# Performance work log

Measured on AMD Instinct MI355X. Metric: run time of the kernel, lower is better.

Reference implementation:

```python
import jax, jax.numpy as jnp
import numpy as np

B, S, H, E, V, OOV = 64, 400, 512, 256, 50000, 100

def setup_inputs() -> dict:
    key = jax.random.key(0)
    ks = jax.random.split(key, 32)
    p = lambda i, shape: jax.random.normal(ks[i], shape, jnp.float32) * 0.02
    emb = p(0, (V, E)).at[0].set(0.0)  # padding_idx=0
    return dict(
        summaries_in=jax.random.randint(ks[1], (B,), 1, V),
        h0=jax.random.normal(ks[2], (B, H), jnp.float32),
        c0=jax.random.normal(ks[3], (B, H), jnp.float32),
        encoder_out=jax.random.normal(ks[4], (B, S, 2 * H), jnp.float32),
        encoder_features=jax.random.normal(ks[5], (S * B, 2 * H), jnp.float32),
        encoder_mask=jnp.ones((S, B), jnp.float32),
        context=jax.random.normal(ks[6], (B, 2 * H), jnp.float32),
        coverage=jax.random.uniform(ks[7], (S, B), jnp.float32) * 0.01,
        texts_extended=jax.random.randint(ks[8], (S, B), 0, V + OOV),
        oov_size=OOV,
        emb=emb,
        W_feat=p(10, (2 * H, 2 * H)), b_feat=p(11, (2 * H,)),
        W_cov=p(12, (2 * H,)), b_cov=p(13, (2 * H,)),
        w_att=p(14, (2 * H,)), b_att=p(15, ()),
        W_ih=p(16, (4 * H, E)), W_hh=p(17, (4 * H, H)),
        b_ih=p(18, (4 * H,)), b_hh=p(19, (4 * H,)),
        W_ctx=p(20, (E, 2 * H + E)), b_ctx=p(21, (E,)),
        W_pg=p(22, (4 * H + E,)), b_pg=p(23, ()),
        W_o1=p(24, (H, 3 * H)), b_o1=p(25, (H,)),
        W_o2=p(26, (V, H)), b_o2=p(27, (V,)),
    )


def reference(summaries_in, h0, c0, encoder_out, encoder_features, encoder_mask,
              context, coverage, texts_extended, oov_size, emb,
              W_feat, b_feat, W_cov, b_cov, w_att, b_att,
              W_ih, W_hh, b_ih, b_hh, W_ctx, b_ctx, W_pg, b_pg,
              W_o1, b_o1, W_o2, b_o2):
    # embedding + context projection: [B, 2H+E] -> [B, E]
    x = emb[summaries_in]
    ctx_out = jnp.concatenate([context, x], axis=1) @ W_ctx.T + b_ctx
    # single LSTM step (torch gate order i, f, g, o)
    gates = ctx_out @ W_ih.T + b_ih + h0 @ W_hh.T + b_hh
    i, f, g, o = jnp.split(gates, 4, axis=1)
    c = jax.nn.sigmoid(f) * c0 + jax.nn.sigmoid(i) * jnp.tanh(g)
    h = jax.nn.sigmoid(o) * jnp.tanh(c)
    hidden_out = jnp.concatenate([h, c], axis=1)  # [B, 2H]
    # Bahdanau attention with coverage
    dec_feat = hidden_out @ W_feat.T + b_feat                 # [B, 2H]
    ef = encoder_features.reshape(S, B, 2 * H)                # [S, B, 2H]
    cov_feat = coverage[..., None] * W_cov + b_cov            # Linear(1, 2H)
    e = jnp.tanh(ef + dec_feat[None] + cov_feat) @ w_att + b_att  # [S, B]
    a = jax.nn.softmax(e, axis=0) * encoder_mask
    a = a / jnp.sum(a, axis=0, keepdims=True)                 # renormalize (Normalize(0))
    ctx_new = jnp.einsum('sb,bsd->bd', a, encoder_out)        # [B, 2H]
    coverage_next = coverage + a
    # pointer-generator mix
    gen_in = jnp.concatenate([ctx_new, hidden_out, ctx_out], axis=1)  # [B, 4H+E]
    p_gen = jax.nn.sigmoid(gen_in @ W_pg + b_pg)[:, None]             # [B, 1]
    logits = (jnp.concatenate([h, ctx_new], axis=1) @ W_o1.T + b_o1) @ W_o2.T + b_o2
    vocab_dist = p_gen * jax.nn.softmax(logits, axis=1)       # [B, V]
    attn_w = (1.0 - p_gen) * a.T                              # [B, S]
    vd = jnp.concatenate([vocab_dist, jnp.zeros((B, oov_size), vocab_dist.dtype)], axis=1)
    vd = vd.at[jnp.arange(B)[:, None], texts_extended.T].add(attn_w)  # scatter_add copy dist
    return vd, hidden_out, ctx_new, a, coverage_next
```

## Files before the change

kernel.cpp:

```cpp
#include <hip/hip_runtime.h>
#include <cmath>

#define B 64
#define S 400
#define H 512
#define E 256
#define V 50000
#define OOV 100
#define H2 1024
#define VDN (V + OOV)
#define NBLK_V 782
#define SC 40

typedef __attribute__((ext_vector_type(8))) short short8;
typedef __attribute__((ext_vector_type(4))) float f32x4;

__device__ __forceinline__ float wred_sum(float v) {
#pragma unroll
  for (int o = 32; o > 0; o >>= 1) v += __shfl_down(v, o, 64);
  return v;
}
__device__ __forceinline__ float wred_max(float v) {
#pragma unroll
  for (int o = 32; o > 0; o >>= 1) v = fmaxf(v, __shfl_down(v, o, 64));
  return v;
}
__device__ __forceinline__ short f2bf(float f) {
  return __builtin_bit_cast(short, (__bf16)f);
}

__global__ __launch_bounds__(256) void k_pre(
    const float* __restrict__ b_ctx, const float* __restrict__ b_ih,
    const float* __restrict__ b_hh, const float* __restrict__ b_feat,
    const float* __restrict__ b_o1, const float* __restrict__ context,
    const float* __restrict__ emb, const int* __restrict__ sumin,
    const float* __restrict__ h0, float* __restrict__ ctxoutT4,
    float* __restrict__ gates, float* __restrict__ dfeat,
    float* __restrict__ innerT4, float* __restrict__ catT4,
    float* __restrict__ h0T4) {
  int idx = blockIdx.x * 256 + threadIdx.x;
  if (idx < 16384) {
    int j = ((idx >> 8) << 2) + (idx & 3);
    ctxoutT4[idx] = b_ctx[j];
  } else if (idx < 16384 + 131072) {
    int i = idx - 16384;
    int j = i & 2047;
    gates[i] = b_ih[j] + b_hh[j];
  } else if (idx < 16384 + 131072 + 65536) {
    int i = idx - 16384 - 131072;
    dfeat[i] = b_feat[i & 1023];
  } else if (idx < 245760) {
    int i = idx - 16384 - 131072 - 65536;
    int j = ((i >> 8) << 2) + (i & 3);
    innerT4[i] = b_o1[j];
  } else if (idx < 245760 + 81920) {
    int i = idx - 245760;
    int e = i & 3, b = (i >> 2) & 63, q = i >> 8;
    int k = q * 4 + e;
    catT4[i] = (k < 1024) ? context[b * 1024 + k]
                          : emb[(size_t)sumin[b] * 256 + (k - 1024)];
  } else {
    int i = idx - 245760 - 81920;
    int e = i & 3, b = (i >> 2) & 63, q = i >> 8;
    h0T4[i] = h0[b * 512 + q * 4 + e];
  }
}

template <int R, int KC, int OUTMODE>
__global__ __launch_bounds__(256) void k_gemmsk(
    const float* __restrict__ A1, const float* __restrict__ W1, int ldw1, int s1,
    const float* __restrict__ A2, const float* __restrict__ W2, int ldw2,
    float* __restrict__ out, int ldout) {
  const int lane = threadIdx.x;
  const int w = threadIdx.y;
  const int j0 = blockIdx.x * (4 * R) + w * R;
  const float* A;
  const float* W;
  int ldw, kc0;
  if ((int)blockIdx.y < s1) {
    A = A1; W = W1; ldw = ldw1; kc0 = blockIdx.y * KC;
  } else {
    A = A2; W = W2; ldw = ldw2; kc0 = (blockIdx.y - s1) * KC;
  }
  float acc[R];
#pragma unroll
  for (int r = 0; r < R; ++r) acc[r] = 0.f;
  const float* ap = A + (size_t)kc0 * 256 + lane * 4;
  const float* wr[R];
#pragma unroll
  for (int r = 0; r < R; ++r) wr[r] = W + (size_t)(j0 + r) * ldw + kc0 * 4;
#pragma unroll 8
  for (int k4 = 0; k4 < KC; ++k4) {
    float4 av = *(const float4*)(ap + (size_t)k4 * 256);
#pragma unroll
    for (int r = 0; r < R; ++r) {
      float4 wv = *(const float4*)(wr[r] + k4 * 4);
      acc[r] += av.x * wv.x + av.y * wv.y + av.z * wv.z + av.w * wv.w;
    }
  }
#pragma unroll
  for (int r = 0; r < R; ++r) {
    int j = j0 + r;
    if constexpr (OUTMODE == 0)
      atomicAdd(&out[((size_t)(j >> 2) * 64 + lane) * 4 + (j & 3)], acc[r]);
    else
      atomicAdd(&out[(size_t)lane * ldout + j], acc[r]);
  }
}

__global__ __launch_bounds__(256) void k_lstm(const float* __restrict__ gates,
                                              const float* __restrict__ c0,
                                              float* __restrict__ hidden,
                                              float* __restrict__ hcT4) {
  int idx = blockIdx.x * 256 + threadIdx.x;
  int b = idx >> 9, u = idx & 511;
  float gi = gates[(size_t)b * 2048 + u];
  float gf = gates[(size_t)b * 2048 + 512 + u];
  float gg = gates[(size_t)b * 2048 + 1024 + u];
  float go = gates[(size_t)b * 2048 + 1536 + u];
  float si = 1.f / (1.f + expf(-gi));
  float sf = 1.f / (1.f + expf(-gf));
  float so = 1.f / (1.f + expf(-go));
  float c = sf * c0[(size_t)b * 512 + u] + si * tanhf(gg);
  float h = so * tanhf(c);
  hidden[(size_t)b * H2 + u] = h;
  hidden[(size_t)b * H2 + 512 + u] = c;
  hcT4[((u >> 2) * 64 + b) * 4 + (u & 3)] = h;
  int k = 512 + u;
  hcT4[((k >> 2) * 64 + b) * 4 + (k & 3)] = c;
}

__global__ __launch_bounds__(256) void k_e(
    const float* __restrict__ ef, const float* __restrict__ dfeat,
    const float* __restrict__ cov, const float* __restrict__ Wcov,
    const float* __restrict__ bcov, const float* __restrict__ watt,
    const float* __restrict__ batt, float* __restrict__ e_out) {
  const int t = threadIdx.x;
  const int r = t >> 5;
  const int li = t & 31;
  const int sb = blockIdx.x * 8 + r;
  const int b = sb & 63;
  const float cval = cov[sb];
  const float4* efr = (const float4*)(ef + (size_t)sb * H2);
  const float4* dfr = (const float4*)(dfeat + (size_t)b * H2);
  const float4* wcr = (const float4*)Wcov;
  const float4* bcr = (const float4*)bcov;
  const float4* war = (const float4*)watt;
  float sum = 0.f;
#pragma unroll
  for (int i = 0; i < 8; ++i) {
    int d4 = li + i * 32;
    float4 ev = efr[d4], dv = dfr[d4], wc = wcr[d4], bc = bcr[d4], wa = war[d4];
    sum += tanhf(ev.x + dv.x + cval * wc.x + bc.x) * wa.x;
    sum += tanhf(ev.y + dv.y + cval * wc.y + bc.y) * wa.y;
    sum += tanhf(ev.z + dv.z + cval * wc.z + bc.z) * wa.z;
    sum += tanhf(ev.w + dv.w + cval * wc.w + bc.w) * wa.w;
  }
#pragma unroll
  for (int o = 16; o > 0; o >>= 1) sum += __shfl_down(sum, o, 32);
  if (li == 0) e_out[sb] = sum + batt[0];
}

__global__ __launch_bounds__(512) void k_soft(const float* __restrict__ e,
                                              const float* __restrict__ mask,
                                              const float* __restrict__ cov_in,
                                              float* __restrict__ a_out,
                                              float* __restrict__ cov_out) {
  const int b = blockIdx.x;
  const int s = threadIdx.x;
  __shared__ float red[8];
  float ev = (s < S) ? e[s * B + b] : -INFINITY;
  float m = wred_max(ev);
  if ((s & 63) == 0) red[s >> 6] = m;
  __syncthreads();
  if (s == 0) {
    float mm = red[0];
#pragma unroll
    for (int i = 1; i < 8; ++i) mm = fmaxf(mm, red[i]);
    red[0] = mm;
  }
  __syncthreads();
  m = red[0];
  float ex = (s < S) ? mask[s * B + b] * expf(ev - m) : 0.f;
  float ws = wred_sum(ex);
  __syncthreads();
  if ((s & 63) == 0) red[s >> 6] = ws;
  __syncthreads();
  if (s == 0) {
    float z = 0.f;
#pragma unroll
    for (int i = 0; i < 8; ++i) z += red[i];
    red[0] = z;
  }
  __syncthreads();
  float Z = red[0];
  if (s < S) {
    float av = ex / Z;
    a_out[s * B + b] = av;
    cov_out[s * B + b] = cov_in[s * B + b] + av;
  }
}

__global__ __launch_bounds__(256) void k_ctxp(const float* __restrict__ a,
                                              const float* __restrict__ enc,
                                              float* __restrict__ part) {
  const int b = blockIdx.x & 63;
  const int sc = blockIdx.x >> 6;
  const int d = threadIdx.x * 4;
  float4 acc = make_float4(0.f, 0.f, 0.f, 0.f);
#pragma unroll
  for (int i = 0; i < 10; ++i) {
    int s = sc * 10 + i;
    float av = a[s * B + b];
    float4 ev = *(const float4*)(enc + ((size_t)b * S + s) * H2 + d);
    acc.x += av * ev.x;
    acc.y += av * ev.y;
    acc.z += av * ev.z;
    acc.w += av * ev.w;
  }
  *(float4*)(part + (size_t)blockIdx.x * H2 + d) = acc;
}

__global__ __launch_bounds__(256) void k_ctxred(const float* __restrict__ part,
                                                float* __restrict__ ctx_new,
                                                float* __restrict__ ctxT4) {
  int idx = blockIdx.x * 256 + threadIdx.x;
  float s = 0.f;
#pragma unroll
  for (int sc = 0; sc < SC; ++sc) s += part[(size_t)sc * 65536 + idx];
  int b = idx >> 10, d = idx & 1023;
  ctx_new[idx] = s;
  ctxT4[((d >> 2) * 64 + b) * 4 + (d & 3)] = s;
}

__global__ __launch_bounds__(256) void k_pgen(
    const float* __restrict__ ctx_new, const float* __restrict__ hidden,
    const float* __restrict__ ctxoutT4, const float* __restrict__ Wpg,
    const float* __restrict__ bpg, float* __restrict__ pgen) {
  const int b = blockIdx.x;
  float p = 0.f;
  for (int k = threadIdx.x; k < 2304; k += 256) {
    float v;
    if (k < 1024) v = ctx_new[(size_t)b * H2 + k];
    else if (k < 2048) v = hidden[(size_t)b * H2 + k - 1024];
    else {
      int ko = k - 2048;
      v = ctxoutT4[((ko >> 2) * 64 + b) * 4 + (ko & 3)];
    }
    p += v * Wpg[k];
  }
  p = wred_sum(p);
  __shared__ float red[4];
  if ((threadIdx.x & 63) == 0) red[threadIdx.x >> 6] = p;
  __syncthreads();
  if (threadIdx.x == 0) {
    float d = red[0] + red[1] + red[2] + red[3] + bpg[0];
    pgen[b] = 1.f / (1.f + expf(-d));
  }
}

__global__ __launch_bounds__(256) void k_packinner(const float* __restrict__ innerT4,
                                                   short8* __restrict__ packB) {
  int f = blockIdx.x * 256 + threadIdx.x;
  int l = f & 63, bt = (f >> 6) & 3, ks = f >> 8;
  int b = bt * 16 + (l & 15);
  int kbase = ks * 32 + (l >> 4) * 8;
  float4 q0 = *(const float4*)&innerT4[(size_t)(kbase / 4) * 256 + b * 4];
  float4 q1 = *(const float4*)&innerT4[(size_t)(kbase / 4 + 1) * 256 + b * 4];
  short8 frag;
  frag[0] = f2bf(q0.x); frag[1] = f2bf(q0.y);
  frag[2] = f2bf(q0.z); frag[3] = f2bf(q0.w);
  frag[4] = f2bf(q1.x); frag[5] = f2bf(q1.y);
  frag[6] = f2bf(q1.z); frag[7] = f2bf(q1.w);
  packB[f] = frag;
}

__global__ __launch_bounds__(256) void k_mfma_logits(
    const float* __restrict__ W2, const short8* __restrict__ packB,
    const float* __restrict__ bias, float* __restrict__ logits,
    float* __restrict__ mp, float* __restrict__ zp) {
  const int l = threadIdx.x;
  const int w = threadIdx.y;
  const int jblk = blockIdx.x * 64;
  const int jw = jblk + w * 16;
  const int jv = min(jw + (l & 15), V - 1);
  const float4* wp4 = (const float4*)(W2 + (size_t)jv * 512 + (l >> 4) * 8);

  f32x4 acc0 = {0.f, 0.f, 0.f, 0.f}, acc1 = acc0, acc2 = acc0, acc3 = acc0;
  float4 cw0 = wp4[0], cw1 = wp4[1];
#pragma unroll
  for (int ks = 0; ks < 16; ++ks) {
    float4 nw0, nw1;
    if (ks < 15) { nw0 = wp4[(ks + 1) * 8]; nw1 = wp4[(ks + 1) * 8 + 1]; }
    short8 af;
    af[0] = f2bf(cw0.x); af[1] = f2bf(cw0.y); af[2] = f2bf(cw0.z); af[3] = f2bf(cw0.w);
    af[4] = f2bf(cw1.x); af[5] = f2bf(cw1.y); af[6] = f2bf(cw1.z); af[7] = f2bf(cw1.w);
    short8 b0 = packB[(ks * 4 + 0) * 64 + l];
    short8 b1 = packB[(ks * 4 + 1) * 64 + l];
    short8 b2 = packB[(ks * 4 + 2) * 64 + l];
    short8 b3 = packB[(ks * 4 + 3) * 64 + l];
    acc0 = __builtin_amdgcn_mfma_f32_16x16x32_bf16(af, b0, acc0, 0, 0, 0);
    acc1 = __builtin_amdgcn_mfma_f32_16x16x32_bf16(af, b1, acc1, 0, 0, 0);
    acc2 = __builtin_amdgcn_mfma_f32_16x16x32_bf16(af, b2, acc2, 0, 0, 0);
    acc3 = __builtin_amdgcn_mfma_f32_16x16x32_bf16(af, b3, acc3, 0, 0, 0);
    if (ks < 15) { cw0 = nw0; cw1 = nw1; }
  }

  __shared__ float tile[64][65];
  const int rbase = w * 16 + (l >> 4) * 4;
#pragma unroll
  for (int v = 0; v < 4; ++v) {
    int jl = rbase + v;
    int j = jblk + jl;
    float bv = bias[min(j, V - 1)];
    bool valid = (j < V);
    tile[jl][0 * 16 + (l & 15)] = valid ? acc0[v] + bv : -INFINITY;
    tile[jl][1 * 16 + (l & 15)] = valid ? acc1[v] + bv : -INFINITY;
    tile[jl][2 * 16 + (l & 15)] = valid ? acc2[v] + bv : -INFINITY;
    tile[jl][3 * 16 + (l & 15)] = valid ? acc3[v] + bv : -INFINITY;
  }
  __syncthreads();
  const int t = w * 64 + l;
#pragma unroll
  for (int i = 0; i < 16; ++i) {
    int idx = i * 256 + t;
    int jl = idx & 63;
    int b = idx >> 6;
    int j = jblk + jl;
    if (j < V) logits[(size_t)b * V + j] = tile[jl][b];
  }
  if (t < 64) {
    float m = -INFINITY;
#pragma unroll
    for (int jl = 0; jl < 64; ++jl) m = fmaxf(m, tile[jl][t]);
    float z = 0.f;
#pragma unroll
    for (int jl = 0; jl < 64; ++jl) z += expf(tile[jl][t] - m);
    mp[(size_t)blockIdx.x * 64 + t] = m;
    zp[(size_t)blockIdx.x * 64 + t] = z;
  }
}

__global__ __launch_bounds__(256) void k_vdm(const float* __restrict__ logits,
                                             const float* __restrict__ mp,
                                             const float* __restrict__ zp,
                                             const float* __restrict__ pgen,
                                             float* __restrict__ out) {
  const int b = blockIdx.x >> 3;
  const int c = blockIdx.x & 7;
  const int t = threadIdx.x;
  __shared__ float red[4];
  float m = -INFINITY;
  for (int i = t; i < NBLK_V; i += 256) m = fmaxf(m, mp[i * 64 + b]);
  m = wred_max(m);
  if ((t & 63) == 0) red[t >> 6] = m;
  __syncthreads();
  const float M = fmaxf(fmaxf(red[0], red[1]), fmaxf(red[2], red[3]));
  float z = 0.f;
  for (int i = t; i < NBLK_V; i += 256) z += zp[i * 64 + b] * expf(mp[i * 64 + b] - M);
  z = wred_sum(z);
  __syncthreads();
  if ((t & 63) == 0) red[t >> 6] = z;
  __syncthreads();
  const float Z = red[0] + red[1] + red[2] + red[3];
  const float scale = pgen[b] / Z;
  const int v0 = c * 6272;
  const int v1 = min(v0 + 6272, VDN);
  for (int v = v0 + t; v < v1; v += 256) {
    float val = (v < V) ? scale * expf(logits[(size_t)b * V + v] - M) : 0.f;
    out[(size_t)b * VDN + v] = val;
  }
}

__global__ __launch_bounds__(256) void k_scatter(const float* __restrict__ a,
                                                 const int* __restrict__ tex,
                                                 const float* __restrict__ pgen,
                                                 float* __restrict__ vd) {
  int g = blockIdx.x * 256 + threadIdx.x;
  if (g >= S * B) return;
  int b = g & 63;
  float w = (1.f - pgen[b]) * a[g];
  atomicAdd(&vd[(size_t)b * VDN + tex[g]], w);
}

extern "C" void kernel_launch(void* const* d_in, const int* in_sizes, int n_in,
                              void* d_out, int out_size, void* d_ws, size_t ws_size,
                              hipStream_t stream) {
  const int* sumin = (const int*)d_in[0];
  const float* h0 = (const float*)d_in[1];
  const float* c0 = (const float*)d_in[2];
  const float* enc_out = (const float*)d_in[3];
  const float* ef = (const float*)d_in[4];
  const float* mask = (const float*)d_in[5];
  const float* context = (const float*)d_in[6];
  const float* coverage = (const float*)d_in[7];
  const int* tex = (const int*)d_in[8];
  const float* emb = (const float*)d_in[10];
  const float* W_feat = (const float*)d_in[11];
  const float* b_feat = (const float*)d_in[12];
  const float* W_cov = (const float*)d_in[13];
  const float* b_cov = (const float*)d_in[14];
  const float* w_att = (const float*)d_in[15];
  const float* b_att = (const float*)d_in[16];
  const float* W_ih = (const float*)d_in[17];
  const float* W_hh = (const float*)d_in[18];
  const float* b_ih = (const float*)d_in[19];
  const float* b_hh = (const float*)d_in[20];
  const float* W_ctx = (const float*)d_in[21];
  const float* b_ctx = (const float*)d_in[22];
  const float* W_pg = (const float*)d_in[23];
  const float* b_pg = (const float*)d_in[24];
  const float* W_o1 = (const float*)d_in[25];
  const float* b_o1 = (const float*)d_in[26];
  const float* W_o2 = (const float*)d_in[27];
  const float* b_o2 = (const float*)d_in[28];

  float* out = (float*)d_out;
  float* vd = out;
  float* hidden = vd + (size_t)B * VDN;
  float* ctx_new = hidden + (size_t)B * H2;
  float* a_out = ctx_new + (size_t)B * H2;
  float* cov_out = a_out + (size_t)S * B;

  float* ws = (float*)d_ws;
  float* catT4 = ws;
  float* h0T4 = catT4 + 81920;
  float* ctxoutT4 = h0T4 + 32768;
  float* gates = ctxoutT4 + 16384;
  float* hidcatT4 = gates + 131072;
  float* dfeat = hidcatT4 + 65536;
  float* e_ws = dfeat + 65536;
  float* ctxnewT4 = e_ws + 25600;
  float* innerT4 = ctxnewT4 + 65536;
  float* pgen = innerT4 + 32768;
  float* mp = pgen + 64;
  float* zp = mp + 50048;
  float* packBf = zp + 50048;
  float* logits = packBf + 16384;
  float* part = logits;
  short8* packB = (short8*)packBf;

  dim3 gblk(64, 4);

  k_pre<<<1408, 256, 0, stream>>>(b_ctx, b_ih, b_hh, b_feat, b_o1, context, emb,
                                  sumin, h0, ctxoutT4, gates, dfeat, innerT4,
                                  catT4, h0T4);
  k_gemmsk<2, 64, 0><<<dim3(32, 5), gblk, 0, stream>>>(
      catT4, W_ctx, 1280, 5, nullptr, nullptr, 0, ctxoutT4, 0);
  k_gemmsk<2, 64, 1><<<dim3(256, 3), gblk, 0, stream>>>(
      ctxoutT4, W_ih, 256, 1, h0T4, W_hh, 512, gates, 2048);
  k_lstm<<<128, 256, 0, stream>>>(gates, c0, hidden, hidcatT4);
  k_gemmsk<2, 64, 1><<<dim3(128, 4), gblk, 0, stream>>>(
      hidcatT4, W_feat, 1024, 4, nullptr, nullptr, 0, dfeat, 1024);
  k_e<<<3200, 256, 0, stream>>>(ef, dfeat, coverage, W_cov, b_cov, w_att, b_att,
                                e_ws);
  k_soft<<<B, 512, 0, stream>>>(e_ws, mask, coverage, a_out, cov_out);
  k_ctxp<<<SC * B, 256, 0, stream>>>(a_out, enc_out, part);
  k_ctxred<<<256, 256, 0, stream>>>(part, ctx_new, ctxnewT4);
  k_pgen<<<B, 256, 0, stream>>>(ctx_new, hidden, ctxoutT4, W_pg, b_pg, pgen);
  k_gemmsk<2, 64, 0><<<dim3(64, 6), gblk, 0, stream>>>(
      hidcatT4, W_o1, 1536, 2, ctxnewT4, W_o1 + 512, 1536, innerT4, 0);
  k_packinner<<<16, 256, 0, stream>>>(innerT4, packB);
  k_mfma_logits<<<NBLK_V, gblk, 0, stream>>>(W_o2, packB, b_o2, logits, mp, zp);
  k_vdm<<<B * 8, 256, 0, stream>>>(logits, mp, zp, pgen, vd);
  k_scatter<<<100, 256, 0, stream>>>(a_out, tex, pgen, vd);
}
```

Measured before the change: 231.7 us.

## Fuse kernel chain into persistent kernels with grid-wide atomic barriers

Collapses about fifteen small launches into four: a front kernel (bias init, ctx projection, LSTM GEMMs and cell, W_feat GEMM), the attention-energy kernel, a mid kernel (softmax, context reduction, pgen, W_o1, pack) and a logits kernel that also does the vocab softmax normalisation, the final write and the scatter. Phases are separated by software grid barriers on atomic counters. The logits tile stays in LDS and the final distribution is written straight from it, so the global logits round trip goes away. tanh, sigmoid and exp also switch to fast intrinsics. This removes launch overhead and one pass over the logits, but relies on all blocks being co-resident (782 blocks in the last kernel) and slightly lowers numeric precision.

Result: slower. 834.1 us (+260.1%).

```diff
diff --git a/kernel.cpp b/kernel.cpp
--- a/kernel.cpp
+++ b/kernel.cpp
@@ -3,14 +3,11 @@
 
 #define B 64
 #define S 400
-#define H 512
-#define E 256
 #define V 50000
 #define OOV 100
 #define H2 1024
 #define VDN (V + OOV)
 #define NBLK_V 782
-#define SC 40
 
 typedef __attribute__((ext_vector_type(8))) short short8;
 typedef __attribute__((ext_vector_type(4))) float f32x4;
@@ -28,106 +25,137 @@
 __device__ __forceinline__ short f2bf(float f) {
   return __builtin_bit_cast(short, (__bf16)f);
 }
-
-__global__ __launch_bounds__(256) void k_pre(
+__device__ __forceinline__ float ftanh(float x) {
+  float e = __expf(2.f * x);
+  return 1.f - 2.f * __builtin_amdgcn_rcpf(e + 1.f);
+}
+
+__device__ __forceinline__ void gbar(unsigned* cnt, int slot, unsigned nblk) {
+  __syncthreads();
+  if (threadIdx.x == 0 && threadIdx.y == 0) {
+    __threadfence();
+    __hip_atomic_fetch_add(cnt + slot * 32, 1u, __ATOMIC_ACQ_REL,
+                           __HIP_MEMORY_SCOPE_AGENT);
+    while (__hip_atomic_load(cnt + slot * 32, __ATOMIC_ACQUIRE,
+                             __HIP_MEMORY_SCOPE_AGENT) < nblk)
+      __builtin_amdgcn_s_sleep(2);
+    __threadfence();
+  }
+  __syncthreads();
+}
+
+__global__ __launch_bounds__(256) void k_zero(unsigned* __restrict__ cnt,
+                                              float* __restrict__ vd) {
+  int t = blockIdx.x * 256 + threadIdx.x;
+  if (t < 2048) cnt[t] = 0u;
+  if (t < B * OOV) {
+    int b = t / OOV, v = t % OOV;
+    vd[(size_t)b * VDN + V + v] = 0.f;
+  }
+}
+
+template <int OM>
+__device__ __forceinline__ void gemm_u(const float* __restrict__ A,
+                                       const float* __restrict__ W, int ldw,
+                                       int kc0, int j0, float* __restrict__ out,
+                                       int ldout, int lane) {
+  float a0 = 0.f, a1 = 0.f;
+  const float* ap = A + (size_t)kc0 * 256 + lane * 4;
+  const float* w0 = W + (size_t)j0 * ldw + kc0 * 4;
+  const float* w1 = w0 + ldw;
+#pragma unroll 8
+  for (int k4 = 0; k4 < 64; ++k4) {
+    float4 av = *(const float4*)(ap + k4 * 256);
+    float4 v0 = *(const float4*)(w0 + k4 * 4);
+    float4 v1 = *(const float4*)(w1 + k4 * 4);
+    a0 += av.x * v0.x + av.y * v0.y + av.z * v0.z + av.w * v0.w;
+    a1 += av.x * v1.x + av.y * v1.y + av.z * v1.z + av.w * v1.w;
+  }
+  if constexpr (OM == 0) {
+    atomicAdd(&out[((size_t)(j0 >> 2) * 64 + lane) * 4 + (j0 & 3)], a0);
+    atomicAdd(&out[((size_t)((j0 + 1) >> 2) * 64 + lane) * 4 + ((j0 + 1) & 3)], a1);
+  } else {
+    atomicAdd(&out[(size_t)lane * ldout + j0], a0);
+    atomicAdd(&out[(size_t)lane * ldout + j0 + 1], a1);
+  }
+}
+
+__global__ __launch_bounds__(256) void k_front(
     const float* __restrict__ b_ctx, const float* __restrict__ b_ih,
     const float* __restrict__ b_hh, const float* __restrict__ b_feat,
     const float* __restrict__ b_o1, const float* __restrict__ context,
     const float* __restrict__ emb, const int* __restrict__ sumin,
-    const float* __restrict__ h0, float* __restrict__ ctxoutT4,
-    float* __restrict__ gates, float* __restrict__ dfeat,
-    float* __restrict__ innerT4, float* __restrict__ catT4,
-    float* __restrict__ h0T4) {
-  int idx = blockIdx.x * 256 + threadIdx.x;
-  if (idx < 16384) {
-    int j = ((idx >> 8) << 2) + (idx & 3);
-    ctxoutT4[idx] = b_ctx[j];
-  } else if (idx < 16384 + 131072) {
-    int i = idx - 16384;
-    int j = i & 2047;
-    gates[i] = b_ih[j] + b_hh[j];
-  } else if (idx < 16384 + 131072 + 65536) {
-    int i = idx - 16384 - 131072;
-    dfeat[i] = b_feat[i & 1023];
-  } else if (idx < 245760) {
-    int i = idx - 16384 - 131072 - 65536;
-    int j = ((i >> 8) << 2) + (i & 3);
-    innerT4[i] = b_o1[j];
-  } else if (idx < 245760 + 81920) {
-    int i = idx - 245760;
-    int e = i & 3, b = (i >> 2) & 63, q = i >> 8;
-    int k = q * 4 + e;
-    catT4[i] = (k < 1024) ? context[b * 1024 + k]
-                          : emb[(size_t)sumin[b] * 256 + (k - 1024)];
-  } else {
-    int i = idx - 245760 - 81920;
-    int e = i & 3, b = (i >> 2) & 63, q = i >> 8;
-    h0T4[i] = h0[b * 512 + q * 4 + e];
-  }
-}
-
-template <int R, int KC, int OUTMODE>
-__global__ __launch_bounds__(256) void k_gemmsk(
-    const float* __restrict__ A1, const float* __restrict__ W1, int ldw1, int s1,
-    const float* __restrict__ A2, const float* __restrict__ W2, int ldw2,
-    float* __restrict__ out, int ldout) {
-  const int lane = threadIdx.x;
-  const int w = threadIdx.y;
-  const int j0 = blockIdx.x * (4 * R) + w * R;
-  const float* A;
-  const float* W;
-  int ldw, kc0;
-  if ((int)blockIdx.y < s1) {
-    A = A1; W = W1; ldw = ldw1; kc0 = blockIdx.y * KC;
-  } else {
-    A = A2; W = W2; ldw = ldw2; kc0 = (blockIdx.y - s1) * KC;
-  }
-  float acc[R];
-#pragma unroll
-  for (int r = 0; r < R; ++r) acc[r] = 0.f;
-  const float* ap = A + (size_t)kc0 * 256 + lane * 4;
-  const float* wr[R];
-#pragma unroll
-  for (int r = 0; r < R; ++r) wr[r] = W + (size_t)(j0 + r) * ldw + kc0 * 4;
-#pragma unroll 8
-  for (int k4 = 0; k4 < KC; ++k4) {
-    float4 av = *(const float4*)(ap + (size_t)k4 * 256);
-#pragma unroll
-    for (int r = 0; r < R; ++r) {
-      float4 wv = *(const float4*)(wr[r] + k4 * 4);
-      acc[r] += av.x * wv.x + av.y * wv.y + av.z * wv.z + av.w * wv.w;
-    }
-  }
-#pragma unroll
-  for (int r = 0; r < R; ++r) {
-    int j = j0 + r;
-    if constexpr (OUTMODE == 0)
-      atomicAdd(&out[((size_t)(j >> 2) * 64 + lane) * 4 + (j & 3)], acc[r]);
+    const float* __restrict__ h0, const float* __restrict__ c0,
+    const float* __restrict__ W_ctx, const float* __restrict__ W_ih,
+    const float* __restrict__ W_hh, const float* __restrict__ W_feat,
+    float* __restrict__ ctxoutT4, float* __restrict__ gates,
+    float* __restrict__ dfeat, float* __restrict__ innerT4,
+    float* __restrict__ catT4, float* __restrict__ h0T4,
+    float* __restrict__ hidden, float* __restrict__ hidcatT4,
+    unsigned* __restrict__ cnt) {
+  const int blk = blockIdx.x, t = threadIdx.x;
+  const int lane = t & 63, w = t >> 6;
+  for (int idx = blk * 256 + t; idx < 360448; idx += 65536) {
+    if (idx < 16384) {
+      int j = ((idx >> 8) << 2) + (idx & 3);
+      ctxoutT4[idx] = b_ctx[j];
+    } else if (idx < 147456) {
+      int i = idx - 16384;
+      gates[i] = b_ih[i & 2047] + b_hh[i & 2047];
+    } else if (idx < 212992) {
+      int i = idx - 147456;
+      dfeat[i] = b_feat[i & 1023];
+    } else if (idx < 245760) {
+      int i = idx - 212992;
+      int j = ((i >> 8) << 2) + (i & 3);
+      innerT4[i] = b_o1[j];
+    } else if (idx < 327680) {
+      int i = idx - 245760;
+      int e = i & 3, bb = (i >> 2) & 63, q = i >> 8;
+      int k = q * 4 + e;
+      catT4[i] = (k < 1024) ? context[bb * 1024 + k]
+                            : emb[(size_t)sumin[bb] * 256 + (k - 1024)];
+    } else {
+      int i = idx - 327680;
+      int e = i & 3, bb = (i >> 2) & 63, q = i >> 8;
+      h0T4[i] = h0[bb * 512 + q * 4 + e];
+    }
+  }
+  gbar(cnt, 0, 256);
+  for (int u = blk; u < 160; u += 256)
+    gemm_u<0>(catT4, W_ctx, 1280, (u / 32) * 64, (u % 32) * 8 + w * 2, ctxoutT4,
+              0, lane);
+  gbar(cnt, 1, 256);
+  for (int u = blk; u < 768; u += 256) {
+    int jb = u & 255, y = u >> 8;
+    if (y == 0)
+      gemm_u<1>(ctxoutT4, W_ih, 256, 0, jb * 8 + w * 2, gates, 2048, lane);
     else
-      atomicAdd(&out[(size_t)lane * ldout + j], acc[r]);
-  }
-}
-
-__global__ __launch_bounds__(256) void k_lstm(const float* __restrict__ gates,
-                                              const float* __restrict__ c0,
-                                              float* __restrict__ hidden,
-                                              float* __restrict__ hcT4) {
-  int idx = blockIdx.x * 256 + threadIdx.x;
-  int b = idx >> 9, u = idx & 511;
-  float gi = gates[(size_t)b * 2048 + u];
-  float gf = gates[(size_t)b * 2048 + 512 + u];
-  float gg = gates[(size_t)b * 2048 + 1024 + u];
-  float go = gates[(size_t)b * 2048 + 1536 + u];
-  float si = 1.f / (1.f + expf(-gi));
-  float sf = 1.f / (1.f + expf(-gf));
-  float so = 1.f / (1.f + expf(-go));
-  float c = sf * c0[(size_t)b * 512 + u] + si * tanhf(gg);
-  float h = so * tanhf(c);
-  hidden[(size_t)b * H2 + u] = h;
-  hidden[(size_t)b * H2 + 512 + u] = c;
-  hcT4[((u >> 2) * 64 + b) * 4 + (u & 3)] = h;
-  int k = 512 + u;
-  hcT4[((k >> 2) * 64 + b) * 4 + (k & 3)] = c;
+      gemm_u<1>(h0T4, W_hh, 512, (y - 1) * 64, jb * 8 + w * 2, gates, 2048, lane);
+  }
+  gbar(cnt, 2, 256);
+  for (int idx = blk * 256 + t; idx < 32768; idx += 65536) {
+    int b = idx >> 9, u = idx & 511;
+    float gi = gates[(size_t)b * 2048 + u];
+    float gf = gates[(size_t)b * 2048 + 512 + u];
+    float gg = gates[(size_t)b * 2048 + 1024 + u];
+    float go = gates[(size_t)b * 2048 + 1536 + u];
+    float si = __builtin_amdgcn_rcpf(1.f + __expf(-gi));
+    float sf = __builtin_amdgcn_rcpf(1.f + __expf(-gf));
+    float so = __builtin_amdgcn_rcpf(1.f + __expf(-go));
+    float c = sf * c0[(size_t)b * 512 + u] + si * ftanh(gg);
+    float h = so * ftanh(c);
+    hidden[(size_t)b * H2 + u] = h;
+    hidden[(size_t)b * H2 + 512 + u] = c;
+    hidcatT4[((u >> 2) * 64 + b) * 4 + (u & 3)] = h;
+    int k = 512 + u;
+    hidcatT4[((k >> 2) * 64 + b) * 4 + (k & 3)] = c;
+  }
+  gbar(cnt, 3, 256);
+  for (int u = blk; u < 512; u += 256) {
+    int jb = u & 127, y = u >> 7;
+    gemm_u<1>(hidcatT4, W_feat, 1024, y * 64, jb * 8 + w * 2, dfeat, 1024, lane);
+  }
 }
 
 __global__ __launch_bounds__(256) void k_e(
@@ -151,236 +179,231 @@
   for (int i = 0; i < 8; ++i) {
     int d4 = li + i * 32;
     float4 ev = efr[d4], dv = dfr[d4], wc = wcr[d4], bc = bcr[d4], wa = war[d4];
-    sum += tanhf(ev.x + dv.x + cval * wc.x + bc.x) * wa.x;
-    sum += tanhf(ev.y + dv.y + cval * wc.y + bc.y) * wa.y;
-    sum += tanhf(ev.z + dv.z + cval * wc.z + bc.z) * wa.z;
-    sum += tanhf(ev.w + dv.w + cval * wc.w + bc.w) * wa.w;
+    sum += ftanh(ev.x + dv.x + cval * wc.x + bc.x) * wa.x;
+    sum += ftanh(ev.y + dv.y + cval * wc.y + bc.y) * wa.y;
+    sum += ftanh(ev.z + dv.z + cval * wc.z + bc.z) * wa.z;
+    sum += ftanh(ev.w + dv.w + cval * wc.w + bc.w) * wa.w;
   }
 #pragma unroll
   for (int o = 16; o > 0; o >>= 1) sum += __shfl_down(sum, o, 32);
   if (li == 0) e_out[sb] = sum + batt[0];
 }
 
-__global__ __launch_bounds__(512) void k_soft(const float* __restrict__ e,
-                                              const float* __restrict__ mask,
-                                              const float* __restrict__ cov_in,
-                                              float* __restrict__ a_out,
-                                              float* __restrict__ cov_out) {
-  const int b = blockIdx.x;
-  const int s = threadIdx.x;
-  __shared__ float red[8];
-  float ev = (s < S) ? e[s * B + b] : -INFINITY;
-  float m = wred_max(ev);
-  if ((s & 63) == 0) red[s >> 6] = m;
-  __syncthreads();
-  if (s == 0) {
-    float mm = red[0];
-#pragma unroll
-    for (int i = 1; i < 8; ++i) mm = fmaxf(mm, red[i]);
-    red[0] = mm;
-  }
-  __syncthreads();
-  m = red[0];
-  float ex = (s < S) ? mask[s * B + b] * expf(ev - m) : 0.f;
-  float ws = wred_sum(ex);
-  __syncthreads();
-  if ((s & 63) == 0) red[s >> 6] = ws;
-  __syncthreads();
-  if (s == 0) {
-    float z = 0.f;
-#pragma unroll
-    for (int i = 0; i < 8; ++i) z += red[i];
-    red[0] = z;
-  }
-  __syncthreads();
-  float Z = red[0];
-  if (s < S) {
-    float av = ex / Z;
-    a_out[s * B + b] = av;
-    cov_out[s * B + b] = cov_in[s * B + b] + av;
-  }
-}
-
-__global__ __launch_bounds__(256) void k_ctxp(const float* __restrict__ a,
-                                              const float* __restrict__ enc,
-                                              float* __restrict__ part) {
-  const int b = blockIdx.x & 63;
-  const int sc = blockIdx.x >> 6;
-  const int d = threadIdx.x * 4;
-  float4 acc = make_float4(0.f, 0.f, 0.f, 0.f);
-#pragma unroll
-  for (int i = 0; i < 10; ++i) {
-    int s = sc * 10 + i;
-    float av = a[s * B + b];
-    float4 ev = *(const float4*)(enc + ((size_t)b * S + s) * H2 + d);
-    acc.x += av * ev.x;
-    acc.y += av * ev.y;
-    acc.z += av * ev.z;
-    acc.w += av * ev.w;
-  }
-  *(float4*)(part + (size_t)blockIdx.x * H2 + d) = acc;
-}
-
-__global__ __launch_bounds__(256) void k_ctxred(const float* __restrict__ part,
-                                                float* __restrict__ ctx_new,
-                                                float* __restrict__ ctxT4) {
-  int idx = blockIdx.x * 256 + threadIdx.x;
-  float s = 0.f;
-#pragma unroll
-  for (int sc = 0; sc < SC; ++sc) s += part[(size_t)sc * 65536 + idx];
-  int b = idx >> 10, d = idx & 1023;
-  ctx_new[idx] = s;
-  ctxT4[((d >> 2) * 64 + b) * 4 + (d & 3)] = s;
-}
-
-__global__ __launch_bounds__(256) void k_pgen(
-    const float* __restrict__ ctx_new, const float* __restrict__ hidden,
-    const float* __restrict__ ctxoutT4, const float* __restrict__ Wpg,
-    const float* __restrict__ bpg, float* __restrict__ pgen) {
-  const int b = blockIdx.x;
-  float p = 0.f;
-  for (int k = threadIdx.x; k < 2304; k += 256) {
-    float v;
-    if (k < 1024) v = ctx_new[(size_t)b * H2 + k];
-    else if (k < 2048) v = hidden[(size_t)b * H2 + k - 1024];
-    else {
-      int ko = k - 2048;
-      v = ctxoutT4[((ko >> 2) * 64 + b) * 4 + (ko & 3)];
-    }
-    p += v * Wpg[k];
-  }
-  p = wred_sum(p);
+__global__ __launch_bounds__(256) void k_mid(
+    const float* __restrict__ e_ws, const float* __restrict__ mask,
+    const float* __restrict__ coverage, const float* __restrict__ enc,
+    const float* __restrict__ Wpg, const float* __restrict__ bpg,
+    const float* __restrict__ W_o1, const float* __restrict__ hidden,
+    const float* __restrict__ ctxoutT4, const float* __restrict__ hidcatT4,
+    float* __restrict__ a_out, float* __restrict__ cov_out,
+    float* __restrict__ part, float* __restrict__ ctx_new,
+    float* __restrict__ ctxnewT4, float* __restrict__ pgen,
+    float* __restrict__ innerT4, short8* __restrict__ packB,
+    unsigned* __restrict__ cnt) {
+  const int blk = blockIdx.x, t = threadIdx.x;
+  const int lane = t & 63, w = t >> 6;
   __shared__ float red[4];
-  if ((threadIdx.x & 63) == 0) red[threadIdx.x >> 6] = p;
-  __syncthreads();
-  if (threadIdx.x == 0) {
-    float d = red[0] + red[1] + red[2] + red[3] + bpg[0];
-    pgen[b] = 1.f / (1.f + expf(-d));
-  }
-}
-
-__global__ __launch_bounds__(256) void k_packinner(const float* __restrict__ innerT4,
-                                                   short8* __restrict__ packB) {
-  int f = blockIdx.x * 256 + threadIdx.x;
-  int l = f & 63, bt = (f >> 6) & 3, ks = f >> 8;
-  int b = bt * 16 + (l & 15);
-  int kbase = ks * 32 + (l >> 4) * 8;
-  float4 q0 = *(const float4*)&innerT4[(size_t)(kbase / 4) * 256 + b * 4];
-  float4 q1 = *(const float4*)&innerT4[(size_t)(kbase / 4 + 1) * 256 + b * 4];
-  short8 frag;
-  frag[0] = f2bf(q0.x); frag[1] = f2bf(q0.y);
-  frag[2] = f2bf(q0.z); frag[3] = f2bf(q0.w);
-  frag[4] = f2bf(q1.x); frag[5] = f2bf(q1.y);
-  frag[6] = f2bf(q1.z); frag[7] = f2bf(q1.w);
-  packB[f] = frag;
-}
-
-__global__ __launch_bounds__(256) void k_mfma_logits(
+  if (blk < 64) {
+    const int b = blk;
+    float e1 = e_ws[t * B + b];
+    float e2 = (t < S - 256) ? e_ws[(t + 256) * B + b] : -INFINITY;
+    float m = wred_max(fmaxf(e1, e2));
+    if (lane == 0) red[w] = m;
+    __syncthreads();
+    float M = fmaxf(fmaxf(red[0], red[1]), fmaxf(red[2], red[3]));
+    __syncthreads();
+    float x1 = mask[t * B + b] * __expf(e1 - M);
+    float x2 = (t < S - 256) ? mask[(t + 256) * B + b] * __expf(e2 - M) : 0.f;
+    float zs = wred_sum(x1 + x2);
+    if (lane == 0) red[w] = zs;
+    __syncthreads();
+    float Z = red[0] + red[1] + red[2] + red[3];
+    float rZ = 1.f / Z;
+    float a1 = x1 * rZ;
+    a_out[t * B + b] = a1;
+    cov_out[t * B + b] = coverage[t * B + b] + a1;
+    if (t < S - 256) {
+      float a2 = x2 * rZ;
+      a_out[(t + 256) * B + b] = a2;
+      cov_out[(t + 256) * B + b] = coverage[(t + 256) * B + b] + a2;
+    }
+  }
+  gbar(cnt, 4, 256);
+  {
+    const int b = blk & 63, q = blk >> 6;
+    const int d = t * 4;
+    float4 acc = make_float4(0.f, 0.f, 0.f, 0.f);
+#pragma unroll 10
+    for (int i = 0; i < 100; ++i) {
+      int s = q * 100 + i;
+      float av = a_out[s * B + b];
+      float4 ev = *(const float4*)(enc + ((size_t)b * S + s) * H2 + d);
+      acc.x += av * ev.x;
+      acc.y += av * ev.y;
+      acc.z += av * ev.z;
+      acc.w += av * ev.w;
+    }
+    *(float4*)(part + (size_t)(q * 64 + b) * H2 + d) = acc;
+  }
+  gbar(cnt, 5, 256);
+  {
+    int idx = blk * 256 + t;
+    float s = part[idx] + part[65536 + idx] + part[131072 + idx] +
+              part[196608 + idx];
+    int b = idx >> 10, d = idx & 1023;
+    ctx_new[idx] = s;
+    ctxnewT4[((d >> 2) * 64 + b) * 4 + (d & 3)] = s;
+  }
+  gbar(cnt, 6, 256);
+  for (int u = blk; u < 448; u += 256) {
+    if (u < 64) {
+      const int b = u;
+      float p = 0.f;
+      for (int k = t; k < 2304; k += 256) {
+        float v;
+        if (k < 1024) v = ctx_new[(size_t)b * H2 + k];
+        else if (k < 2048) v = hidden[(size_t)b * H2 + k - 1024];
+        else {
+          int ko = k - 2048;
+          v = ctxoutT4[((ko >> 2) * 64 + b) * 4 + (ko & 3)];
+        }
+        p += v * Wpg[k];
+      }
+      p = wred_sum(p);
+      if (lane == 0) red[w] = p;
+      __syncthreads();
+      if (t == 0) {
+        float dd = red[0] + red[1] + red[2] + red[3] + bpg[0];
+        pgen[b] = 1.f / (1.f + __expf(-dd));
+      }
+      __syncthreads();
+    } else {
+      int v = u - 64;
+      int jb = v & 63, y = v >> 6;
+      if (y < 2)
+        gemm_u<0>(hidcatT4, W_o1, 1536, y * 64, jb * 8 + w * 2, innerT4, 0, lane);
+      else
+        gemm_u<0>(ctxnewT4, W_o1 + 512, 1536, (y - 2) * 64, jb * 8 + w * 2,
+                  innerT4, 0, lane);
+    }
+  }
+  gbar(cnt, 7, 256);
+  if (blk < 16) {
+    int f = blk * 256 + t;
+    int l = f & 63, bt = (f >> 6) & 3, ks = f >> 8;
+    int b = bt * 16 + (l & 15);
+    int kbase = ks * 32 + (l >> 4) * 8;
+    float4 q0 = *(const float4*)&innerT4[(size_t)(kbase / 4) * 256 + b * 4];
+    float4 q1 = *(const float4*)&innerT4[(size_t)(kbase / 4 + 1) * 256 + b * 4];
+    short8 frag;
+    frag[0] = f2bf(q0.x); frag[1] = f2bf(q0.y);
+    frag[2] = f2bf(q0.z); frag[3] = f2bf(q0.w);
+    frag[4] = f2bf(q1.x); frag[5] = f2bf(q1.y);
+    frag[6] = f2bf(q1.z); frag[7] = f2bf(q1.w);
+    packB[f] = frag;
+  }
+}
+
+__global__ __launch_bounds__(256) void k_mfma(
     const float* __restrict__ W2, const short8* __restrict__ packB,
-    const float* __restrict__ bias, float* __restrict__ logits,
-    float* __restrict__ mp, float* __restrict__ zp) {
+    const float* __restrict__ bias, const float* __restrict__ pgen,
+    const float* __restrict__ a_out, const int* __restrict__ tex,
+    float* __restrict__ mp, float* __restrict__ zp, float* __restrict__ mz,
+    float* __restrict__ vd, unsigned* __restrict__ cnt) {
   const int l = threadIdx.x;
   const int w = threadIdx.y;
+  const int t = w * 64 + l;
   const int jblk = blockIdx.x * 64;
-  const int jw = jblk + w * 16;
-  const int jv = min(jw + (l & 15), V - 1);
-  const float4* wp4 = (const float4*)(W2 + (size_t)jv * 512 + (l >> 4) * 8);
-
-  f32x4 acc0 = {0.f, 0.f, 0.f, 0.f}, acc1 = acc0, acc2 = acc0, acc3 = acc0;
-  float4 cw0 = wp4[0], cw1 = wp4[1];
-#pragma unroll
-  for (int ks = 0; ks < 16; ++ks) {
-    float4 nw0, nw1;
-    if (ks < 15) { nw0 = wp4[(ks + 1) * 8]; nw1 = wp4[(ks + 1) * 8 + 1]; }
-    short8 af;
-    af[0] = f2bf(cw0.x); af[1] = f2bf(cw0.y); af[2] = f2bf(cw0.z); af[3] = f2bf(cw0.w);
-    af[4] = f2bf(cw1.x); af[5] = f2bf(cw1.y); af[6] = f2bf(cw1.z); af[7] = f2bf(cw1.w);
-    short8 b0 = packB[(ks * 4 + 0) * 64 + l];
-    short8 b1 = packB[(ks * 4 + 1) * 64 + l];
-    short8 b2 = packB[(ks * 4 + 2) * 64 + l];
-    short8 b3 = packB[(ks * 4 + 3) * 64 + l];
-    acc0 = __builtin_amdgcn_mfma_f32_16x16x32_bf16(af, b0, acc0, 0, 0, 0);
-    acc1 = __builtin_amdgcn_mfma_f32_16x16x32_bf16(af, b1, acc1, 0, 0, 0);
-    acc2 = __builtin_amdgcn_mfma_f32_16x16x32_bf16(af, b2, acc2, 0, 0, 0);
-    acc3 = __builtin_amdgcn_mfma_f32_16x16x32_bf16(af, b3, acc3, 0, 0, 0);
-    if (ks < 15) { cw0 = nw0; cw1 = nw1; }
-  }
-
   __shared__ float tile[64][65];
-  const int rbase = w * 16 + (l >> 4) * 4;
-#pragma unroll
-  for (int v = 0; v < 4; ++v) {
-    int jl = rbase + v;
-    int j = jblk + jl;
-    float bv = bias[min(j, V - 1)];
-    bool valid = (j < V);
-    tile[jl][0 * 16 + (l & 15)] = valid ? acc0[v] + bv : -INFINITY;
-    tile[jl][1 * 16 + (l & 15)] = valid ? acc1[v] + bv : -INFINITY;
-    tile[jl][2 * 16 + (l & 15)] = valid ? acc2[v] + bv : -INFINITY;
-    tile[jl][3 * 16 + (l & 15)] = valid ? acc3[v] + bv : -INFINITY;
-  }
-  __syncthreads();
-  const int t = w * 64 + l;
+  {
+    const int jv = min(jblk + w * 16 + (l & 15), V - 1);
+    const float4* wp4 = (const float4*)(W2 + (size_t)jv * 512 + (l >> 4) * 8);
+    f32x4 acc0 = {0.f, 0.f, 0.f, 0.f}, acc1 = acc0, acc2 = acc0, acc3 = acc0;
+    float4 cw0 = wp4[0], cw1 = wp4[1];
+#pragma unroll
+    for (int ks = 0; ks < 16; ++ks) {
+      float4 nw0, nw1;
+      if (ks < 15) { nw0 = wp4[(ks + 1) * 8]; nw1 = wp4[(ks + 1) * 8 + 1]; }
+      short8 af;
+      af[0] = f2bf(cw0.x); af[1] = f2bf(cw0.y);
+      af[2] = f2bf(cw0.z); af[3] = f2bf(cw0.w);
+      af[4] = f2bf(cw1.x); af[5] = f2bf(cw1.y);
+      af[6] = f2bf(cw1.z); af[7] = f2bf(cw1.w);
+      short8 b0 = packB[(ks * 4 + 0) * 64 + l];
+      short8 b1 = packB[(ks * 4 + 1) * 64 + l];
+      short8 b2 = packB[(ks * 4 + 2) * 64 + l];
+      short8 b3 = packB[(ks * 4 + 3) * 64 + l];
+      acc0 = __builtin_amdgcn_mfma_f32_16x16x32_bf16(af, b0, acc0, 0, 0, 0);
+      acc1 = __builtin_amdgcn_mfma_f32_16x16x32_bf16(af, b1, acc1, 0, 0, 0);
+      acc2 = __builtin_amdgcn_mfma_f32_16x16x32_bf16(af, b2, acc2, 0, 0, 0);
+      acc3 = __builtin_amdgcn_mfma_f32_16x16x32_bf16(af, b3, acc3, 0, 0, 0);
+      if (ks < 15) { cw0 = nw0; cw1 = nw1; }
+    }
+    const int rbase = w * 16 + (l >> 4) * 4;
+#pragma unroll
+    for (int v = 0; v < 4; ++v) {
+      int jl = rbase + v;
+      int j = jblk + jl;
+      float bv = bias[min(j, V - 1)];
+      bool valid = (j < V);
+      tile[jl][0 * 16 + (l & 15)] = valid ? acc0[v] + bv : -INFINITY;
+      tile[jl][1 * 16 + (l & 15)] = valid ? acc1[v] + bv : -INFINITY;
+      tile[jl][2 * 16 + (l & 15)] = valid ? acc2[v] + bv : -INFINITY;
+      tile[jl][3 * 16 + (l & 15)] = valid ? acc3[v] + bv : -INFINITY;
+    }
+    __syncthreads();
+    if (t < 64) {
+      float m = -INFINITY;
+#pragma unroll
+      for (int jl = 0; jl < 64; ++jl) m = fmaxf(m, tile[jl][t]);
+      float z = 0.f;
+#pragma unroll
+      for (int jl = 0; jl < 64; ++jl) z += __expf(tile[jl][t] - m);
+      mp[(size_t)blockIdx.x * 64 + t] = m;
+      zp[(size_t)blockIdx.x * 64 + t] = z;
+    }
+  }
+  gbar(cnt, 8, NBLK_V);
+  if ((int)blockIdx.x < 64) {
+    const int b = blockIdx.x;
+    __shared__ float red2[4];
+    float m = -INFINITY;
+    for (int i = t; i < NBLK_V; i += 256) m = fmaxf(m, mp[i * 64 + b]);
+    m = wred_max(m);
+    if (l == 0) red2[w] = m;
+    __syncthreads();
+    float M = fmaxf(fmaxf(red2[0], red2[1]), fmaxf(red2[2], red2[3]));
+    __syncthreads();
+    float z = 0.f;
+    for (int i = t; i < NBLK_V; i += 256)
+      z += zp[i * 64 + b] * __expf(mp[i * 64 + b] - M);
+    z = wred_sum(z);
+    if (l == 0) red2[w] = z;
+    __syncthreads();
+    if (t == 0) {
+      mz[b] = M;
+      mz[64 + b] = pgen[b] / (red2[0] + red2[1] + red2[2] + red2[3]);
+    }
+  }
+  gbar(cnt, 9, NBLK_V);
 #pragma unroll
   for (int i = 0; i < 16; ++i) {
     int idx = i * 256 + t;
     int jl = idx & 63;
     int b = idx >> 6;
     int j = jblk + jl;
-    if (j < V) logits[(size_t)b * V + j] = tile[jl][b];
-  }
-  if (t < 64) {
-    float m = -INFINITY;
-#pragma unroll
-    for (int jl = 0; jl < 64; ++jl) m = fmaxf(m, tile[jl][t]);
-    float z = 0.f;
-#pragma unroll
-    for (int jl = 0; jl < 64; ++jl) z += expf(tile[jl][t] - m);
-    mp[(size_t)blockIdx.x * 64 + t] = m;
-    zp[(size_t)blockIdx.x * 64 + t] = z;
-  }
-}
-
-__global__ __launch_bounds__(256) void k_vdm(const float* __restrict__ logits,
-                                             const float* __restrict__ mp,
-                                             const float* __restrict__ zp,
-                                             const float* __restrict__ pgen,
-                                             float* __restrict__ out) {
-  const int b = blockIdx.x >> 3;
-  const int c = blockIdx.x & 7;
-  const int t = threadIdx.x;
-  __shared__ float red[4];
-  float m = -INFINITY;
-  for (int i = t; i < NBLK_V; i += 256) m = fmaxf(m, mp[i * 64 + b]);
-  m = wred_max(m);
-  if ((t & 63) == 0) red[t >> 6] = m;
-  __syncthreads();
-  const float M = fmaxf(fmaxf(red[0], red[1]), fmaxf(red[2], red[3]));
-  float z = 0.f;
-  for (int i = t; i < NBLK_V; i += 256) z += zp[i * 64 + b] * expf(mp[i * 64 + b] - M);
-  z = wred_sum(z);
-  __syncthreads();
-  if ((t & 63) == 0) red[t >> 6] = z;
-  __syncthreads();
-  const float Z = red[0] + red[1] + red[2] + red[3];
-  const float scale = pgen[b] / Z;
-  const int v0 = c * 6272;
-  const int v1 = min(v0 + 6272, VDN);
-  for (int v = v0 + t; v < v1; v += 256) {
-    float val = (v < V) ? scale * expf(logits[(size_t)b * V + v] - M) : 0.f;
-    out[(size_t)b * VDN + v] = val;
-  }
-}
-
-__global__ __launch_bounds__(256) void k_scatter(const float* __restrict__ a,
-                                                 const int* __restrict__ tex,
-                                                 const float* __restrict__ pgen,
-                                                 float* __restrict__ vd) {
-  int g = blockIdx.x * 256 + threadIdx.x;
-  if (g >= S * B) return;
-  int b = g & 63;
-  float w = (1.f - pgen[b]) * a[g];
-  atomicAdd(&vd[(size_t)b * VDN + tex[g]], w);
+    if (j < V)
+      vd[(size_t)b * VDN + j] = mz[64 + b] * __expf(tile[jl][b] - mz[b]);
+  }
+  gbar(cnt, 10, NBLK_V);
+  if ((int)blockIdx.x < 100) {
+    int g = blockIdx.x * 256 + t;
+    if (g < S * B) {
+      int b = g & 63;
+      float wgt = (1.f - pgen[b]) * a_out[g];
+      atomicAdd(&vd[(size_t)b * VDN + tex[g]], wgt);
+    }
+  }
 }
 
 extern "C" void kernel_launch(void* const* d_in, const int* in_sizes, int n_in,
@@ -435,33 +458,24 @@
   float* pgen = innerT4 + 32768;
   float* mp = pgen + 64;
   float* zp = mp + 50048;
-  float* packBf = zp + 50048;
-  float* logits = packBf + 16384;
-  float* part = logits;
+  float* mz = zp + 50048;
+  float* packBf = mz + 128;
+  float* part = packBf + 16384;
+  unsigned* cnt = (unsigned*)(part + 262144);
   short8* packB = (short8*)packBf;
 
-  dim3 gblk(64, 4);
-
-  k_pre<<<1408, 256, 0, stream>>>(b_ctx, b_ih, b_hh, b_feat, b_o1, context, emb,
-                                  sumin, h0, ctxoutT4, gates, dfeat, innerT4,
-                                  catT4, h0T4);
-  k_gemmsk<2, 64, 0><<<dim3(32, 5), gblk, 0, stream>>>(
-      catT4, W_ctx, 1280, 5, nullptr, nullptr, 0, ctxoutT4, 0);
-  k_gemmsk<2, 64, 1><<<dim3(256, 3), gblk, 0, stream>>>(
-      ctxoutT4, W_ih, 256, 1, h0T4, W_hh, 512, gates, 2048);
-  k_lstm<<<128, 256, 0, stream>>>(gates, c0, hidden, hidcatT4);
-  k_gemmsk<2, 64, 1><<<dim3(128, 4), gblk, 0, stream>>>(
-      hidcatT4, W_feat, 1024, 4, nullptr, nullptr, 0, dfeat, 1024);
+  k_zero<<<25, 256, 0, stream>>>(cnt, vd);
+  k_front<<<256, 256, 0, stream>>>(b_ctx, b_ih, b_hh, b_feat, b_o1, context,
+                                   emb, sumin, h0, c0, W_ctx, W_ih, W_hh,
+                                   W_feat, ctxoutT4, gates, dfeat, innerT4,
+                                   catT4, h0T4, hidden, hidcatT4, cnt);
   k_e<<<3200, 256, 0, stream>>>(ef, dfeat, coverage, W_cov, b_cov, w_att, b_att,
                                 e_ws);
-  k_soft<<<B, 512, 0, stream>>>(e_ws, mask, coverage, a_out, cov_out);
-  k_ctxp<<<SC * B, 256, 0, stream>>>(a_out, enc_out, part);
-  k_ctxred<<<256, 256, 0, stream>>>(part, ctx_new, ctxnewT4);
-  k_pgen<<<B, 256, 0, stream>>>(ctx_new, hidden, ctxoutT4, W_pg, b_pg, pgen);
-  k_gemmsk<2, 64, 0><<<dim3(64, 6), gblk, 0, stream>>>(
-      hidcatT4, W_o1, 1536, 2, ctxnewT4, W_o1 + 512, 1536, innerT4, 0);
-  k_packinner<<<16, 256, 0, stream>>>(innerT4, packB);
-  k_mfma_logits<<<NBLK_V, gblk, 0, stream>>>(W_o2, packB, b_o2, logits, mp, zp);
-  k_vdm<<<B * 8, 256, 0, stream>>>(logits, mp, zp, pgen, vd);
-  k_scatter<<<100, 256, 0, stream>>>(a_out, tex, pgen, vd);
-}
+  k_mid<<<256, 256, 0, stream>>>(e_ws, mask, coverage, enc_out, W_pg, b_pg,
+                                 W_o1, hidden, ctxoutT4, hidcatT4, a_out,
+                                 cov_out, part, ctx_new, ctxnewT4, pgen,
+                                 innerT4, packB, cnt);
+  k_mfma<<<dim3(NBLK_V), dim3(64, 4), 0, stream>>>(W_o2, packB, b_o2, pgen,
+                                                   a_out, tex, mp, zp, mz, vd,
+                                                   cnt);
+}
```
